# Performance work log

Measured on AMD Instinct MI355X. Metric: run time of the kernel, lower is better.

Reference implementation:

```python
import jax, jax.numpy as jnp
import numpy as np

B, T, D, H = 32, 1024, 256, 256


def setup_inputs() -> dict:
    key = jax.random.key(0)
    ks = jax.random.split(key, 11)
    x = jax.random.normal(ks[0], (B, T, D), dtype=jnp.float32)
    len_x = jax.random.randint(ks[1], (B,), 1, T + 1).astype(jnp.int32)

    def xavier(k, fan_in, fan_out):
        return (jax.random.normal(k, (fan_out, fan_in)) * np.sqrt(2.0 / (fan_in + fan_out))).astype(jnp.float32)

    def unif(k, fan_in, shape):
        bound = 1.0 / np.sqrt(fan_in)
        return jax.random.uniform(k, shape, minval=-bound, maxval=bound).astype(jnp.float32)

    return {
        "x": x, "len_x": len_x,
        "Ww1_w": xavier(ks[2], D, H), "Ww1_b": unif(ks[3], D, (H,)),
        "Ww2_w": unif(ks[4], H, (D, H)), "Ww2_b": unif(ks[5], H, (D,)),
        "Wb1_w": xavier(ks[6], D, H), "Wb1_b": unif(ks[7], D, (H,)),
        "Wb2_w": unif(ks[8], H, (D, H)), "Wb2_b": unif(ks[9], H, (D,)),
    }


def _mlp(c, w1, b1, w2, b2):
    h = jax.nn.gelu(c @ w1.T + b1, approximate=False)
    return h @ w2.T + b2


def _ragged_dft(z, lengths, inverse):
    # z: [B, T, D] complex64; per-sample DFT over the first lengths[i] steps.
    t = z.shape[1]
    n = jnp.arange(t)
    kn = (n[:, None] * n[None, :]).astype(jnp.float32)          # [T, T]
    l = lengths.astype(jnp.float32)[:, None, None]               # [B, 1, 1]
    sign = 1.0 if inverse else -1.0
    ang = sign * 2.0 * jnp.pi * kn[None, :, :] / l               # [B, T, T]
    valid = n[None, :] < lengths[:, None]                        # [B, T]
    mask = (valid[:, :, None] & valid[:, None, :]).astype(jnp.float32)
    Wm = jnp.exp(1j * ang).astype(jnp.complex64) * mask
    if inverse:
        Wm = Wm / l.astype(jnp.complex64)
    return jnp.einsum("bkn,bnd->bkd", Wm, z)


def _crelu(z):
    mag = jnp.abs(z)
    phase = jnp.angle(z)
    recomposed = (mag * jnp.exp(1j * phase)).astype(jnp.complex64)
    return jnp.where(mag > 0, recomposed, jnp.zeros((), jnp.complex64))


def reference(x, len_x, Ww1_w, Ww1_b, Ww2_w, Ww2_b, Wb1_w, Wb1_b, Wb2_w, Wb2_b):
    # mean over valid length (torch sums over full T; padding assumed zero-filled contributes)
    c = jnp.sum(x, axis=1) / len_x.astype(x.dtype)[:, None]      # [B, D]
    x_freq = _ragged_dft(x.astype(jnp.complex64), len_x, inverse=False)
    W = _mlp(c, Ww1_w, Ww1_b, Ww2_w, Ww2_b).astype(jnp.complex64)  # [B, D]
    b = _mlp(c, Wb1_w, Wb1_b, Wb2_w, Wb2_b).astype(jnp.complex64)  # [B, D]
    filtered = x_freq * (1.0 + W[:, None, :]) + b[:, None, :]
    activated = _crelu(filtered)
    x_recon = _ragged_dft(activated, len_x, inverse=True)
    return x_recon.real.astype(x.dtype)
```

## Files before the change

kernel.cpp:

```cpp
#include <hip/hip_runtime.h>
#include <math.h>

#define BB 32
#define TT 1024
#define DD 256
#define NBLK1 1024
#define CHUNKS_PER_B 32


__global__ __launch_bounds__(256)
void k_partial(const float* __restrict__ x, float* __restrict__ partial) {
    __shared__ float4 red[4][64];
    const int g    = blockIdx.x;
    const int tid  = threadIdx.x;
    const int wave = tid >> 6;
    const int lane = tid & 63;
    const int row0 = g * 32;

    const float4* xr = (const float4*)(x + (size_t)(row0 + wave * 8) * DD);
    float4 s; s.x = 0.f; s.y = 0.f; s.z = 0.f; s.w = 0.f;
#pragma unroll
    for (int r = 0; r < 8; ++r) {
        float4 v = xr[(size_t)r * 64 + lane];
        s.x += v.x; s.y += v.y; s.z += v.z; s.w += v.w;
    }
    red[wave][lane] = s;
    __syncthreads();
    if (tid < 64) {
        float4 a = red[0][tid], b = red[1][tid], c = red[2][tid], d = red[3][tid];
        float4 o;
        o.x = (a.x + b.x) + (c.x + d.x);
        o.y = (a.y + b.y) + (c.y + d.y);
        o.z = (a.z + b.z) + (c.z + d.z);
        o.w = (a.w + b.w) + (c.w + d.w);
        ((float4*)(partial + (size_t)g * DD))[tid] = o;
    }
}

__global__ __launch_bounds__(256)
void k_mlp(const float* __restrict__ partial, const int* __restrict__ len,
           const float* __restrict__ Ww1_w, const float* __restrict__ Ww1_b,
           const float* __restrict__ Ww2_w, const float* __restrict__ Ww2_b,
           const float* __restrict__ Wb1_w, const float* __restrict__ Wb1_b,
           const float* __restrict__ Wb2_w, const float* __restrict__ Wb2_b,
           float* __restrict__ Wout, float* __restrict__ Bout) {
    __shared__ float csh[DD];
    __shared__ float hsh[DD];
    const int tid = threadIdx.x;
    const int b   = blockIdx.x >> 1;
    const int mlp = blockIdx.x & 1;

    {
        float s = 0.f;
        const float* pp = partial + (size_t)(b * CHUNKS_PER_B) * DD + tid;
#pragma unroll
        for (int ch = 0; ch < CHUNKS_PER_B; ++ch) s += pp[(size_t)ch * DD];
        csh[tid] = s / (float)len[b];
    }
    __syncthreads();
    const float* w1 = mlp ? Wb1_w : Ww1_w;
    const float* b1 = mlp ? Wb1_b : Ww1_b;
    const float* w2 = mlp ? Wb2_w : Ww2_w;
    const float* b2 = mlp ? Wb2_b : Ww2_b;
    float* op       = mlp ? Bout  : Wout;
    {
        const float4* wr = (const float4*)(w1 + (size_t)tid * DD);
        const float4* cc = (const float4*)csh;
        float s = 0.f;
#pragma unroll 8
        for (int k = 0; k < 64; ++k) {
            float4 w = wr[k];
            float4 c4 = cc[k];
            s += w.x * c4.x + w.y * c4.y + w.z * c4.z + w.w * c4.w;
        }
        float v = s + b1[tid];
        hsh[tid] = 0.5f * v * (1.0f + erff(v * 0.70710678118654752440f));
    }
    __syncthreads();
    {
        const float4* wr = (const float4*)(w2 + (size_t)tid * DD);
        const float4* hh = (const float4*)hsh;
        float s = 0.f;
#pragma unroll 8
        for (int k = 0; k < 64; ++k) {
            float4 w = wr[k];
            float4 h4 = hh[k];
            s += w.x * h4.x + w.y * h4.y + w.z * h4.z + w.w * h4.w;
        }
        op[b * DD + tid] = s + b2[tid];
    }
}

__global__ __launch_bounds__(256)
void k_apply(const float* __restrict__ x, const int* __restrict__ len,
             const float* __restrict__ Wf, const float* __restrict__ Bf,
             float* __restrict__ out) {
    const int row  = blockIdx.x * 4 + (threadIdx.x >> 6);
    const int lane = threadIdx.x & 63;
    const int b = row >> 10;
    const int t = row & (TT - 1);
    const int L = len[b];
    const size_t base = (size_t)row * DD;
    float4* o4 = (float4*)(out + base);
    if (t >= L) {
        float4 z; z.x = 0.f; z.y = 0.f; z.z = 0.f; z.w = 0.f;
        o4[lane] = z;
        return;
    }
    float4 x4 = ((const float4*)(x + base))[lane];
    float4 w4 = ((const float4*)(Wf + b * DD))[lane];
    float4 r;
    r.x = x4.x + w4.x * x4.x;
    r.y = x4.y + w4.y * x4.y;
    r.z = x4.z + w4.z * x4.z;
    r.w = x4.w + w4.w * x4.w;
    if (t == 0) {
        float4 b4 = ((const float4*)(Bf + b * DD))[lane];
        r.x += b4.x; r.y += b4.y; r.z += b4.z; r.w += b4.w;
    }
    o4[lane] = r;
}

extern "C" void kernel_launch(void* const* d_in, const int* in_sizes, int n_in,
                              void* d_out, int out_size, void* d_ws, size_t ws_size,
                              hipStream_t stream) {
    const float* x     = (const float*)d_in[0];
    const int*   len   = (const int*)d_in[1];
    const float* Ww1_w = (const float*)d_in[2];
    const float* Ww1_b = (const float*)d_in[3];
    const float* Ww2_w = (const float*)d_in[4];
    const float* Ww2_b = (const float*)d_in[5];
    const float* Wb1_w = (const float*)d_in[6];
    const float* Wb1_b = (const float*)d_in[7];
    const float* Wb2_w = (const float*)d_in[8];
    const float* Wb2_b = (const float*)d_in[9];
    float* out = (float*)d_out;

    float* ws      = (float*)d_ws;
    float* partial = ws;
    float* Wout    = ws + 262144;
    float* Bout    = ws + 270336;

    k_partial<<<NBLK1, 256, 0, stream>>>(x, partial);
    k_mlp<<<2 * BB, 256, 0, stream>>>(partial, len,
                                      Ww1_w, Ww1_b, Ww2_w, Ww2_b,
                                      Wb1_w, Wb1_b, Wb2_w, Wb2_b,
                                      Wout, Bout);
    k_apply<<<BB * TT / 4, 256, 0, stream>>>(x, len, Wout, Bout, out);
}
```

Baseline: 117.8 us.

## Fuse partial-sum and MLP kernels via per-batch release/acquire flags

Merges the column-sum kernel and the MLP kernel into one launch. Each block publishes its partial sum with a release-stored magic flag. The last two chunk blocks of each batch spin on those flags, then each computes one of the two MLPs. The flags are cleared in the following apply kernel so they are ready for the next call. This removes one kernel launch and its dependency gap, at the cost of spin-waiting blocks that assume all producer blocks are co-resident.

```diff
diff --git a/kernel.cpp b/kernel.cpp
--- a/kernel.cpp
+++ b/kernel.cpp
@@ -7,15 +7,27 @@
 #define NBLK1 1024
 #define CHUNKS_PER_B 32
 
+#define FLAG_MAGIC 0xA5B4C3D21F2E3D4CULL
+
 
 __global__ __launch_bounds__(256)
-void k_partial(const float* __restrict__ x, float* __restrict__ partial) {
+void k_partial_mlp(const float* __restrict__ x, const int* __restrict__ len,
+                   const float* __restrict__ Ww1_w, const float* __restrict__ Ww1_b,
+                   const float* __restrict__ Ww2_w, const float* __restrict__ Ww2_b,
+                   const float* __restrict__ Wb1_w, const float* __restrict__ Wb1_b,
+                   const float* __restrict__ Wb2_w, const float* __restrict__ Wb2_b,
+                   float* __restrict__ partial, unsigned long long* __restrict__ flags,
+                   float* __restrict__ Wout, float* __restrict__ Bout) {
     __shared__ float4 red[4][64];
+    __shared__ float csh[DD];
+    __shared__ float hsh[DD];
     const int g    = blockIdx.x;
     const int tid  = threadIdx.x;
     const int wave = tid >> 6;
     const int lane = tid & 63;
     const int row0 = g * 32;
+    const int b    = g >> 5;
+    const int j    = g & 31;
 
     const float4* xr = (const float4*)(x + (size_t)(row0 + wave * 8) * DD);
     float4 s; s.x = 0.f; s.y = 0.f; s.z = 0.f; s.w = 0.f;
@@ -27,37 +39,42 @@
     red[wave][lane] = s;
     __syncthreads();
     if (tid < 64) {
-        float4 a = red[0][tid], b = red[1][tid], c = red[2][tid], d = red[3][tid];
+        float4 a = red[0][tid], b4 = red[1][tid], c4 = red[2][tid], d4 = red[3][tid];
         float4 o;
-        o.x = (a.x + b.x) + (c.x + d.x);
-        o.y = (a.y + b.y) + (c.y + d.y);
-        o.z = (a.z + b.z) + (c.z + d.z);
-        o.w = (a.w + b.w) + (c.w + d.w);
+        o.x = (a.x + b4.x) + (c4.x + d4.x);
+        o.y = (a.y + b4.y) + (c4.y + d4.y);
+        o.z = (a.z + b4.z) + (c4.z + d4.z);
+        o.w = (a.w + b4.w) + (c4.w + d4.w);
         ((float4*)(partial + (size_t)g * DD))[tid] = o;
     }
-}
+    __syncthreads();
 
-__global__ __launch_bounds__(256)
-void k_mlp(const float* __restrict__ partial, const int* __restrict__ len,
-           const float* __restrict__ Ww1_w, const float* __restrict__ Ww1_b,
-           const float* __restrict__ Ww2_w, const float* __restrict__ Ww2_b,
-           const float* __restrict__ Wb1_w, const float* __restrict__ Wb1_b,
-           const float* __restrict__ Wb2_w, const float* __restrict__ Wb2_b,
-           float* __restrict__ Wout, float* __restrict__ Bout) {
-    __shared__ float csh[DD];
-    __shared__ float hsh[DD];
-    const int tid = threadIdx.x;
-    const int b   = blockIdx.x >> 1;
-    const int mlp = blockIdx.x & 1;
+    if (tid == 0) {
+        __threadfence();
+        __hip_atomic_store(&flags[g], (unsigned long long)FLAG_MAGIC,
+                           __ATOMIC_RELEASE, __HIP_MEMORY_SCOPE_AGENT);
+    }
+
+    if (j < 30) return;
+
+    if (tid < 32) {
+        const unsigned long long* fb = flags + b * CHUNKS_PER_B;
+        while (__hip_atomic_load(&fb[tid], __ATOMIC_ACQUIRE,
+                                 __HIP_MEMORY_SCOPE_AGENT) != (unsigned long long)FLAG_MAGIC) { }
+    }
+    __syncthreads();
+    __threadfence();
 
     {
-        float s = 0.f;
+        float sc = 0.f;
         const float* pp = partial + (size_t)(b * CHUNKS_PER_B) * DD + tid;
 #pragma unroll
-        for (int ch = 0; ch < CHUNKS_PER_B; ++ch) s += pp[(size_t)ch * DD];
-        csh[tid] = s / (float)len[b];
+        for (int ch = 0; ch < CHUNKS_PER_B; ++ch) sc += pp[(size_t)ch * DD];
+        csh[tid] = sc / (float)len[b];
     }
     __syncthreads();
+
+    const int mlp   = j & 1;
     const float* w1 = mlp ? Wb1_w : Ww1_w;
     const float* b1 = mlp ? Wb1_b : Ww1_b;
     const float* w2 = mlp ? Wb2_w : Ww2_w;
@@ -66,35 +83,37 @@
     {
         const float4* wr = (const float4*)(w1 + (size_t)tid * DD);
         const float4* cc = (const float4*)csh;
-        float s = 0.f;
+        float sum = 0.f;
 #pragma unroll 8
         for (int k = 0; k < 64; ++k) {
             float4 w = wr[k];
             float4 c4 = cc[k];
-            s += w.x * c4.x + w.y * c4.y + w.z * c4.z + w.w * c4.w;
+            sum += w.x * c4.x + w.y * c4.y + w.z * c4.z + w.w * c4.w;
         }
-        float v = s + b1[tid];
+        float v = sum + b1[tid];
         hsh[tid] = 0.5f * v * (1.0f + erff(v * 0.70710678118654752440f));
     }
     __syncthreads();
     {
         const float4* wr = (const float4*)(w2 + (size_t)tid * DD);
         const float4* hh = (const float4*)hsh;
-        float s = 0.f;
+        float sum = 0.f;
 #pragma unroll 8
         for (int k = 0; k < 64; ++k) {
             float4 w = wr[k];
             float4 h4 = hh[k];
-            s += w.x * h4.x + w.y * h4.y + w.z * h4.z + w.w * h4.w;
+            sum += w.x * h4.x + w.y * h4.y + w.z * h4.z + w.w * h4.w;
         }
-        op[b * DD + tid] = s + b2[tid];
+        op[b * DD + tid] = sum + b2[tid];
     }
 }
 
 __global__ __launch_bounds__(256)
 void k_apply(const float* __restrict__ x, const int* __restrict__ len,
              const float* __restrict__ Wf, const float* __restrict__ Bf,
+             unsigned long long* __restrict__ flags,
              float* __restrict__ out) {
+    if (threadIdx.x == 0 && blockIdx.x < NBLK1) flags[blockIdx.x] = 0ULL;
     const int row  = blockIdx.x * 4 + (threadIdx.x >> 6);
     const int lane = threadIdx.x & 63;
     const int b = row >> 10;
@@ -138,13 +157,13 @@
 
     float* ws      = (float*)d_ws;
     float* partial = ws;
-    float* Wout    = ws + 262144;
-    float* Bout    = ws + 270336;
+    unsigned long long* flags = (unsigned long long*)(ws + 262144);
+    float* Wout    = ws + 262144 + 2048;
+    float* Bout    = Wout + 8192;
 
-    k_partial<<<NBLK1, 256, 0, stream>>>(x, partial);
-    k_mlp<<<2 * BB, 256, 0, stream>>>(partial, len,
-                                      Ww1_w, Ww1_b, Ww2_w, Ww2_b,
-                                      Wb1_w, Wb1_b, Wb2_w, Wb2_b,
-                                      Wout, Bout);
-    k_apply<<<BB * TT / 4, 256, 0, stream>>>(x, len, Wout, Bout, out);
+    k_partial_mlp<<<NBLK1, 256, 0, stream>>>(x, len,
+                                             Ww1_w, Ww1_b, Ww2_w, Ww2_b,
+                                             Wb1_w, Wb1_b, Wb2_w, Wb2_b,
+                                             partial, flags, Wout, Bout);
+    k_apply<<<BB * TT / 4, 256, 0, stream>>>(x, len, Wout, Bout, flags, out);
 }
```

Result: slower. 212.9 us (+80.7%).
